# Kernel tuning notes

Measured on AMD Instinct MI355X. Metric: run time of the kernel, lower is better.

## Reference

```python
import jax, jax.numpy as jnp
import numpy as np
from jax import lax

DIM = 256
HEADS = 8
C3 = DIM * 3 // 4  # 192
C1 = DIM // 4      # 64


def conv1x1(x, w):
    # x: [b,c,h,w], w: [o,c] (1x1 conv, no bias)
    return jnp.einsum('bchw,oc->bohw', x, w)


def dwconv3x3(x, w):
    # x: [b,c,h,w], w: [c,1,3,3] depthwise
    return lax.conv_general_dilated(
        x, w, window_strides=(1, 1), padding='SAME',
        feature_group_count=x.shape[1],
        dimension_numbers=('NCHW', 'OIHW', 'NCHW'))


def l2norm(x, eps=1e-12):
    # torch F.normalize: x / max(||x||, eps) along last dim
    n = jnp.sqrt(jnp.sum(x * x, axis=-1, keepdims=True))
    return x / jnp.maximum(n, eps)


def setup_inputs() -> dict:
    key = jax.random.key(0)
    ks = jax.random.split(key, 10)
    s = 0.02
    return {
        'x': jax.random.normal(ks[0], (4, DIM, 128, 128), jnp.float32),
        'k_v': jax.random.normal(ks[1], (4, 256), jnp.float32),
        'temperature': jnp.ones((HEADS, 1, 1), jnp.float32),
        'w_kR': jax.random.normal(ks[2], (C3, 192), jnp.float32) * s,
        'w_kI': jax.random.normal(ks[3], (C1, 64), jnp.float32) * s,
        'w_qR': jax.random.normal(ks[4], (DIM, C3), jnp.float32) * s,
        'w_qdw': jax.random.normal(ks[5], (DIM, 1, 3, 3), jnp.float32) * s,
        'w_kvI': jax.random.normal(ks[6], (2 * DIM, C1), jnp.float32) * s,
        'w_kvdw': jax.random.normal(ks[7], (2 * DIM, 1, 3, 3), jnp.float32) * s,
        'w_proj': jax.random.normal(ks[8], (DIM, DIM), jnp.float32) * s,
    }


def reference(x, k_v, temperature, w_kR, w_kI, w_qR, w_qdw, w_kvI, w_kvdw, w_proj):
    b, c, h, w = x.shape
    # FiLM-style modulation: x * kv + x
    kvr = (k_v[:, :192] @ w_kR.T)[:, :, None, None]  # [b, C3, 1, 1]
    kvi = (k_v[:, 192:] @ w_kI.T)[:, :, None, None]  # [b, C1, 1, 1]
    x_r = x[:, :C3] * kvr + x[:, :C3]
    x_i = x[:, C3:] * kvi + x[:, C3:]
    # QKV projections
    q = dwconv3x3(conv1x1(x_r, w_qR), w_qdw)          # [b, dim, h, w]
    kv = dwconv3x3(conv1x1(x_i, w_kvI), w_kvdw)       # [b, 2*dim, h, w]
    k, v = jnp.split(kv, 2, axis=1)
    hd = DIM // HEADS
    hw = h * w
    q = q.reshape(b, HEADS, hd, hw)
    k = k.reshape(b, HEADS, hd, hw)
    v = v.reshape(b, HEADS, hd, hw)
    # channel-wise (transposed) attention with L2 norm + temperature
    q = l2norm(q)
    k = l2norm(k)
    attn = jnp.einsum('bhcn,bhdn->bhcd', q, k) * temperature  # [b,H,hd,hd]
    attn = jax.nn.softmax(attn, axis=-1)
    out = jnp.einsum('bhcd,bhdn->bhcn', attn, v)
    out = out.reshape(b, DIM, h, w)
    return conv1x1(out, w_proj)
```

## Files before the change

kernel.cpp:

```cpp
#include <hip/hip_runtime.h>
#include <math.h>

#define HW 16384

typedef unsigned int uint;
typedef short bfrag __attribute__((ext_vector_type(8)));
typedef float f32x4 __attribute__((ext_vector_type(4)));

union FragCvt { uint4 u; bfrag v; };

__device__ inline uint pack2bf(float a, float b) {
  uint ua = __builtin_bit_cast(uint, a);
  uint ub = __builtin_bit_cast(uint, b);
  ua = (ua + 0x7FFFu + ((ua >> 16) & 1u)) >> 16;
  ub = (ub + 0x7FFFu + ((ub >> 16) & 1u)) & 0xFFFF0000u;
  return ua | ub;
}

__device__ inline void cvt_hilo(float4 a, float4 b, bfrag& hi, bfrag& lo) {
  float v0[8] = {a.x, a.y, a.z, a.w, b.x, b.y, b.z, b.w};
  uint hv[4], lv[4];
  #pragma unroll
  for (int i = 0; i < 4; ++i) {
    float x0 = v0[2 * i], x1 = v0[2 * i + 1];
    uint h = pack2bf(x0, x1);
    float h0 = __builtin_bit_cast(float, h << 16);
    float h1 = __builtin_bit_cast(float, h & 0xFFFF0000u);
    hv[i] = h;
    lv[i] = pack2bf(x0 - h0, x1 - h1);
  }
  FragCvt ch, cl;
  ch.u = make_uint4(hv[0], hv[1], hv[2], hv[3]);
  cl.u = make_uint4(lv[0], lv[1], lv[2], lv[3]);
  hi = ch.v;
  lo = cl.v;
}

#define LDS_BARRIER() do { \
  asm volatile("s_waitcnt lgkmcnt(0)" ::: "memory"); \
  __builtin_amdgcn_s_barrier(); \
} while (0)

__global__ __launch_bounds__(256) void mod_kernel(
    const float* __restrict__ kv, const float* __restrict__ wkR,
    const float* __restrict__ wkI, float* __restrict__ mod)
{
  int b = blockIdx.x;
  int c = threadIdx.x;
  const float* kvb = kv + b * 256;
  float s = 0.f;
  if (c < 192) {
    const float* wr = wkR + c * 192;
    for (int j = 0; j < 192; ++j) s += kvb[j] * wr[j];
  } else {
    const float* wi = wkI + (c - 192) * 64;
    for (int j = 0; j < 64; ++j) s += kvb[192 + j] * wi[j];
  }
  mod[b * 256 + c] = 1.f + s;
}

__device__ __forceinline__ void mgemm_body(
    const float* __restrict__ Wt, int ldW,
    const float* __restrict__ Xt,
    const float* __restrict__ modc,
    float* __restrict__ Yt,
    int K, int t, unsigned short* Al, unsigned short* Bl, float* Ml)
{
  int w = t >> 6, l = t & 63;
  int wm = (w >> 1) * 64, wn = (w & 1) * 64;
  int lm = l & 15, lk = (l >> 4) * 8;

  int am = t >> 1, ako = (t & 1) * 16;
  int bn = t & 127, bo = (t >> 7) * 8;

  Ml[t] = (modc && t < K) ? modc[t] : 1.f;

  f32x4 acc[4][4];
  #pragma unroll
  for (int fi = 0; fi < 4; ++fi)
    #pragma unroll
    for (int fj = 0; fj < 4; ++fj) acc[fi][fj] = {0.f, 0.f, 0.f, 0.f};

  float xrA[16], xrB[16];
  float4 wv0, wv1, wv2, wv3;

  auto load_x = [&](float* xr, int k0) {
    #pragma unroll
    for (int i = 0; i < 2; ++i) {
      int kb = k0 + bo + i * 16;
      #pragma unroll
      for (int r = 0; r < 8; ++r)
        xr[i * 8 + r] = Xt[(size_t)(kb + r) * HW + bn];
    }
  };
  auto load_w = [&](int k0) {
    const float* wsrc = Wt + (size_t)am * ldW + k0 + ako;
    wv0 = *(const float4*)(wsrc);
    wv1 = *(const float4*)(wsrc + 4);
    wv2 = *(const float4*)(wsrc + 8);
    wv3 = *(const float4*)(wsrc + 12);
  };
  auto pack_a = [&]() {
    uint4 aw0, aw1;
    aw0.x = pack2bf(wv0.x, wv0.y); aw0.y = pack2bf(wv0.z, wv0.w);
    aw0.z = pack2bf(wv1.x, wv1.y); aw0.w = pack2bf(wv1.z, wv1.w);
    aw1.x = pack2bf(wv2.x, wv2.y); aw1.y = pack2bf(wv2.z, wv2.w);
    aw1.z = pack2bf(wv3.x, wv3.y); aw1.w = pack2bf(wv3.z, wv3.w);
    *(uint4*)&Al[am * 40 + ako] = aw0;
    *(uint4*)&Al[am * 40 + ako + 8] = aw1;
  };
  auto pack_b = [&](const float* xr, int k0) {
    #pragma unroll
    for (int i = 0; i < 2; ++i) {
      float4 m0 = *(const float4*)&Ml[k0 + bo + i * 16];
      float4 m1 = *(const float4*)&Ml[k0 + bo + i * 16 + 4];
      uint4 bw;
      bw.x = pack2bf(xr[i * 8 + 0] * m0.x, xr[i * 8 + 1] * m0.y);
      bw.y = pack2bf(xr[i * 8 + 2] * m0.z, xr[i * 8 + 3] * m0.w);
      bw.z = pack2bf(xr[i * 8 + 4] * m1.x, xr[i * 8 + 5] * m1.y);
      bw.w = pack2bf(xr[i * 8 + 6] * m1.z, xr[i * 8 + 7] * m1.w);
      *(uint4*)&Bl[bn * 40 + bo + i * 16] = bw;
    }
  };
  auto mfma_step = [&]() {
    bfrag af[4], bfr[4];
    #pragma unroll
    for (int fj = 0; fj < 4; ++fj) {
      FragCvt cv;
      cv.u = *(const uint4*)&Al[(wm + fj * 16 + lm) * 40 + lk];
      af[fj] = cv.v;
    }
    #pragma unroll
    for (int fi = 0; fi < 4; ++fi) {
      FragCvt cv;
      cv.u = *(const uint4*)&Bl[(wn + fi * 16 + lm) * 40 + lk];
      bfr[fi] = cv.v;
    }
    #pragma unroll
    for (int fi = 0; fi < 4; ++fi)
      #pragma unroll
      for (int fj = 0; fj < 4; ++fj)
        acc[fi][fj] = __builtin_amdgcn_mfma_f32_16x16x32_bf16(
            bfr[fi], af[fj], acc[fi][fj], 0, 0, 0);
  };

  load_x(xrA, 0);
  load_x(xrB, 32);
  load_w(0);

  for (int k0 = 0; k0 < K; k0 += 64) {
    LDS_BARRIER();
    pack_a();
    if (k0 + 32 < K) load_w(k0 + 32);
    pack_b(xrA, k0);
    if (k0 + 64 < K) load_x(xrA, k0 + 64);
    LDS_BARRIER();
    mfma_step();

    LDS_BARRIER();
    pack_a();
    if (k0 + 64 < K) load_w(k0 + 64);
    pack_b(xrB, k0 + 32);
    if (k0 + 96 < K) load_x(xrB, k0 + 96);
    LDS_BARRIER();
    mfma_step();
  }

  int ph = (l >> 4) * 4;
  #pragma unroll
  for (int fi = 0; fi < 4; ++fi)
    #pragma unroll
    for (int fj = 0; fj < 4; ++fj)
      *(f32x4*)&Yt[(size_t)(wm + fj * 16 + lm) * HW + wn + fi * 16 + ph] =
          acc[fi][fj];
}

__global__ __launch_bounds__(256, 2) void mgemm(
    const float* __restrict__ W, int ldW, size_t Wbstride,
    const float* __restrict__ X, int c0, size_t Xbstride,
    const float* __restrict__ mod,
    float* __restrict__ Y, size_t Ybstride, int K)
{
  __shared__ unsigned short Al[128 * 40];
  __shared__ unsigned short Bl[128 * 40];
  __shared__ float Ml[256];
  int b = blockIdx.z, mt = blockIdx.y, nt = blockIdx.x;
  mgemm_body(W + (size_t)b * Wbstride + (size_t)mt * 128 * ldW, ldW,
             X + (size_t)b * Xbstride + (size_t)c0 * HW + nt * 128,
             mod ? mod + b * 256 + c0 : (const float*)nullptr,
             Y + (size_t)b * Ybstride + (size_t)mt * 128 * HW + nt * 128,
             K, threadIdx.x, Al, Bl, Ml);
}

__global__ __launch_bounds__(256, 2) void mgemm_qk(
    const float* __restrict__ wqR, const float* __restrict__ wkvI,
    const float* __restrict__ X, const float* __restrict__ mod,
    float* __restrict__ Yq, float* __restrict__ Yk)
{
  __shared__ unsigned short Al[128 * 40];
  __shared__ unsigned short Bl[128 * 40];
  __shared__ float Ml[256];
  int b = blockIdx.z, mt = blockIdx.y, nt = blockIdx.x;
  if (mt < 2) {
    mgemm_body(wqR + (size_t)mt * 128 * 192, 192,
               X + (size_t)b * 4194304 + nt * 128,
               mod + b * 256,
               Yq + (size_t)b * 4194304 + (size_t)mt * 128 * HW + nt * 128,
               192, threadIdx.x, Al, Bl, Ml);
  } else {
    int m2 = mt - 2;
    mgemm_body(wkvI + (size_t)m2 * 128 * 64, 64,
               X + (size_t)b * 4194304 + (size_t)192 * HW + nt * 128,
               mod + b * 256 + 192,
               Yk + (size_t)b * 4194304 + (size_t)m2 * 128 * HW + nt * 128,
               64, threadIdx.x, Al, Bl, Ml);
  }
}

__global__ __launch_bounds__(256) void dwconv_kernel(
    const float* __restrict__ in, size_t in_bstride,
    const float* __restrict__ wdw,
    float* __restrict__ out, size_t out_bstride,
    float* __restrict__ ssq)
{
  int c = blockIdx.x;
  int b = blockIdx.y;
  int t = threadIdx.x;
  int r = t >> 5;
  int xq = t & 31;

  const float4* ip4 = (const float4*)(in + (size_t)b * in_bstride + ((size_t)c << 14));
  float4* op4 = (float4*)(out + (size_t)b * out_bstride + ((size_t)c << 14));
  const float* wp = wdw + c * 9;
  float w0 = wp[0], w1 = wp[1], w2 = wp[2], w3 = wp[3], w4 = wp[4],
        w5 = wp[5], w6 = wp[6], w7 = wp[7], w8 = wp[8];

  const float4 z4 = make_float4(0.f, 0.f, 0.f, 0.f);
  int y0 = r << 4;

  float4 a = (y0 > 0) ? ip4[((y0 - 1) << 5) + xq] : z4;
  float4 bb = ip4[(y0 << 5) + xq];

  float aL = __shfl_up(a.w, 1);  if (xq == 0)  aL = 0.f;
  float aR = __shfl_down(a.x, 1); if (xq == 31) aR = 0.f;
  float bL = __shfl_up(bb.w, 1); if (xq == 0)  bL = 0.f;
  float bR = __shfl_down(bb.x, 1); if (xq == 31) bR = 0.f;

  float ss = 0.f;
  #pragma unroll
  for (int i = 0; i < 16; ++i) {
    int y = y0 + i;
    int yc = (y + 1 < 128) ? (y + 1) : 127;
    float4 cc = ip4[(yc << 5) + xq];
    if (y + 1 >= 128) { cc.x = 0.f; cc.y = 0.f; cc.z = 0.f; cc.w = 0.f; }
    float cL = __shfl_up(cc.w, 1);  if (xq == 0)  cL = 0.f;
    float cR = __shfl_down(cc.x, 1); if (xq == 31) cR = 0.f;

    float4 o;
    o.x = w0 * aL  + w1 * a.x + w2 * a.y +
          w3 * bL  + w4 * bb.x + w5 * bb.y +
          w6 * cL  + w7 * cc.x + w8 * cc.y;
    o.y = w0 * a.x + w1 * a.y + w2 * a.z +
          w3 * bb.x + w4 * bb.y + w5 * bb.z +
          w6 * cc.x + w7 * cc.y + w8 * cc.z;
    o.z = w0 * a.y + w1 * a.z + w2 * a.w +
          w3 * bb.y + w4 * bb.z + w5 * bb.w +
          w6 * cc.y + w7 * cc.z + w8 * cc.w;
    o.w = w0 * a.z + w1 * a.w + w2 * aR +
          w3 * bb.z + w4 * bb.w + w5 * bR +
          w6 * cc.z + w7 * cc.w + w8 * cR;

    op4[(y << 5) + xq] = o;
    ss += o.x * o.x + o.y * o.y + o.z * o.z + o.w * o.w;

    a = bb; aL = bL; aR = bR;
    bb = cc; bL = cL; bR = cR;
  }

  if (ssq) {
    #pragma unroll
    for (int off = 32; off > 0; off >>= 1) ss += __shfl_down(ss, off);
    __shared__ float red[4];
    if ((t & 63) == 0) red[t >> 6] = ss;
    __syncthreads();
    if (t == 0) ssq[b * 256 + c] = red[0] + red[1] + red[2] + red[3];
  }
}

__global__ __launch_bounds__(256) void gram_kernel(
    const float* __restrict__ qdw, const float* __restrict__ kdw,
    float* __restrict__ S)
{
  int chunk = blockIdx.x, h = blockIdx.y, b = blockIdx.z;
  int t = threadIdx.x;
  int w = t >> 6, l = t & 63;
  int lm = l & 15;
  int lk8 = (l >> 4) * 8;

  const float* qh = qdw + (((size_t)b * 256 + h * 32) << 14);
  const float* kh = kdw + (((size_t)b * 256 + h * 32) << 14);
  const float* q0 = qh + ((size_t)lm << 14);
  const float* q1 = q0 + ((size_t)16 << 14);
  const float* k0 = kh + ((size_t)lm << 14);
  const float* k1 = k0 + ((size_t)16 << 14);

  int px0 = chunk * 1024 + w * 256 + lk8;

  f32x4 acc[2][2], accl[2][2];
  #pragma unroll
  for (int mi = 0; mi < 2; ++mi)
    #pragma unroll
    for (int nj = 0; nj < 2; ++nj) {
      acc[mi][nj] = {0.f, 0.f, 0.f, 0.f};
      accl[mi][nj] = {0.f, 0.f, 0.f, 0.f};
    }

  #pragma unroll 2
  for (int s = 0; s < 8; ++s) {
    int px = px0 + s * 32;
    float4 a0 = *(const float4*)(q0 + px);
    float4 a1 = *(const float4*)(q0 + px + 4);
    float4 a2 = *(const float4*)(q1 + px);
    float4 a3 = *(const float4*)(q1 + px + 4);
    float4 b0 = *(const float4*)(k0 + px);
    float4 b1 = *(const float4*)(k0 + px + 4);
    float4 b2 = *(const float4*)(k1 + px);
    float4 b3 = *(const float4*)(k1 + px + 4);

    bfrag qhF[2], qlF[2], khF[2], klF[2];
    cvt_hilo(a0, a1, qhF[0], qlF[0]);
    cvt_hilo(a2, a3, qhF[1], qlF[1]);
    cvt_hilo(b0, b1, khF[0], klF[0]);
    cvt_hilo(b2, b3, khF[1], klF[1]);

    #pragma unroll
    for (int mi = 0; mi < 2; ++mi)
      #pragma unroll
      for (int nj = 0; nj < 2; ++nj) {
        acc[mi][nj] = __builtin_amdgcn_mfma_f32_16x16x32_bf16(
            qhF[mi], khF[nj], acc[mi][nj], 0, 0, 0);
        accl[mi][nj] = __builtin_amdgcn_mfma_f32_16x16x32_bf16(
            qhF[mi], klF[nj], accl[mi][nj], 0, 0, 0);
        accl[mi][nj] = __builtin_amdgcn_mfma_f32_16x16x32_bf16(
            qlF[mi], khF[nj], accl[mi][nj], 0, 0, 0);
      }
  }

  __shared__ float red[4][1024];
  int orow = (l >> 4) * 4;
  #pragma unroll
  for (int mi = 0; mi < 2; ++mi)
    #pragma unroll
    for (int nj = 0; nj < 2; ++nj)
      #pragma unroll
      for (int r = 0; r < 4; ++r)
        red[w][(mi * 16 + orow + r) * 32 + nj * 16 + lm] =
            acc[mi][nj][r] + accl[mi][nj][r];
  __syncthreads();
  float* Sp = S + (((size_t)b * 8 + h) << 10);
  for (int idx = t; idx < 1024; idx += 256)
    atomicAdd(&Sp[idx], red[0][idx] + red[1][idx] + red[2][idx] + red[3][idx]);
}

__global__ __launch_bounds__(64) void softmax_kernel(
    float* __restrict__ S, const float* __restrict__ ssq,
    const float* __restrict__ ssk, const float* __restrict__ temp)
{
  int bh = blockIdx.x;
  int b = bh >> 3, h = bh & 7;
  int c = threadIdx.x;
  if (c >= 32) return;
  float* row = S + ((size_t)bh << 10) + c * 32;
  float invq = 1.f / fmaxf(sqrtf(ssq[b * 256 + h * 32 + c]), 1e-12f);
  float T = temp[h];
  float lg[32];
  float mx = -1e30f;
  for (int d = 0; d < 32; ++d) {
    float invk = 1.f / fmaxf(sqrtf(ssk[b * 256 + h * 32 + d]), 1e-12f);
    float v = row[d] * invq * invk * T;
    lg[d] = v;
    mx = fmaxf(mx, v);
  }
  float sum = 0.f;
  for (int d = 0; d < 32; ++d) { float e = expf(lg[d] - mx); lg[d] = e; sum += e; }
  float inv = 1.f / sum;
  for (int d = 0; d < 32; ++d) row[d] = lg[d] * inv;
}

__global__ __launch_bounds__(256) void mbuild_kernel(
    const float* __restrict__ attn, const float* __restrict__ wproj,
    float* __restrict__ M)
{
  int o = blockIdx.x, b = blockIdx.y;
  int col = threadIdx.x;
  int h = col >> 5, d = col & 31;
  const float* a = attn + (((size_t)b * 8 + h) << 10);
  const float* wp = wproj + o * 256 + h * 32;
  float s = 0.f;
  #pragma unroll
  for (int cc = 0; cc < 32; ++cc) s += wp[cc] * a[cc * 32 + d];
  M[((size_t)b * 256 + o) * 256 + col] = s;
}

extern "C" void kernel_launch(void* const* d_in, const int* in_sizes, int n_in,
                              void* d_out, int out_size, void* d_ws, size_t ws_size,
                              hipStream_t stream)
{
  const float* x      = (const float*)d_in[0];
  const float* k_v    = (const float*)d_in[1];
  const float* temp   = (const float*)d_in[2];
  const float* w_kR   = (const float*)d_in[3];
  const float* w_kI   = (const float*)d_in[4];
  const float* w_qR   = (const float*)d_in[5];
  const float* w_qdw  = (const float*)d_in[6];
  const float* w_kvI  = (const float*)d_in[7];
  const float* w_kvdw = (const float*)d_in[8];
  const float* w_proj = (const float*)d_in[9];
  float* out = (float*)d_out;

  float* ws   = (float*)d_ws;
  float* bufA = ws;
  float* bufB = ws + 16777216;
  float* bufC = ws + 33554432;
  float* sm   = ws + 50331648;
  float* mod  = sm;
  float* ssq  = sm + 1024;
  float* ssk  = sm + 2048;
  float* S    = sm + 3072;
  float* M    = sm + 3072 + 32768;

  hipMemsetAsync(S, 0, (size_t)32768 * sizeof(float), stream);

  mod_kernel<<<dim3(4), dim3(256), 0, stream>>>(k_v, w_kR, w_kI, mod);

  mgemm_qk<<<dim3(128, 4, 4), dim3(256), 0, stream>>>(
      w_qR, w_kvI, x, mod, bufA, bufB);

  dwconv_kernel<<<dim3(256, 4), dim3(256), 0, stream>>>(
      bufB, 4194304, w_kvdw, bufC, 4194304, ssk);

  dwconv_kernel<<<dim3(256, 4), dim3(256), 0, stream>>>(
      bufA, 4194304, w_qdw, bufB, 4194304, ssq);

  gram_kernel<<<dim3(16, 8, 4), dim3(256), 0, stream>>>(bufB, bufC, S);

  mgemm<<<dim3(128, 2, 4), dim3(256), 0, stream>>>(
      w_kvI + 256 * 64, 64, 0, x, 192, 4194304, mod, bufA, 4194304, 64);

  softmax_kernel<<<dim3(32), dim3(64), 0, stream>>>(S, ssq, ssk, temp);
  mbuild_kernel<<<dim3(256, 4), dim3(256), 0, stream>>>(S, w_proj, M);

  dwconv_kernel<<<dim3(256, 4), dim3(256), 0, stream>>>(
      bufA, 4194304, w_kvdw + 256 * 9, bufC, 4194304, (float*)nullptr);

  mgemm<<<dim3(128, 2, 4), dim3(256), 0, stream>>>(
      M, 256, 65536, bufC, 0, 4194304, (const float*)nullptr, out, 4194304, 256);
}
```

Baseline: 322.7 us.

## Fuse q/k depthwise convolutions and L2 norm sums into the gram kernel

The two depthwise 3x3 convolutions on q and k are computed inside the gram kernel. Each wave now handles one image row and convolves 8-pixel strips directly from the pre-conv buffers, so the dwconv outputs never need to be written to and re-read from memory. The per-channel sum of squares is accumulated in registers and added to ssq/ssk atomically, and one memset now clears those buffers along with S. In exchange, every pre-conv element is loaded three times (once per stencil row, mostly hitting cache), register pressure goes up, and the grid doubles to 32 chunks.

```diff
diff --git a/kernel.cpp b/kernel.cpp
--- a/kernel.cpp
+++ b/kernel.cpp
@@ -287,24 +287,34 @@
   }
 }
 
-__global__ __launch_bounds__(256) void gram_kernel(
-    const float* __restrict__ qdw, const float* __restrict__ kdw,
-    float* __restrict__ S)
+__global__ __launch_bounds__(256, 3) void gram_fused(
+    const float* __restrict__ qpre, const float* __restrict__ kpre,
+    const float* __restrict__ wqdw, const float* __restrict__ wkdw,
+    float* __restrict__ S, float* __restrict__ ssq, float* __restrict__ ssk)
 {
   int chunk = blockIdx.x, h = blockIdx.y, b = blockIdx.z;
   int t = threadIdx.x;
   int w = t >> 6, l = t & 63;
-  int lm = l & 15;
-  int lk8 = (l >> 4) * 8;
-
-  const float* qh = qdw + (((size_t)b * 256 + h * 32) << 14);
-  const float* kh = kdw + (((size_t)b * 256 + h * 32) << 14);
-  const float* q0 = qh + ((size_t)lm << 14);
-  const float* q1 = q0 + ((size_t)16 << 14);
-  const float* k0 = kh + ((size_t)lm << 14);
-  const float* k1 = k0 + ((size_t)16 << 14);
-
-  int px0 = chunk * 1024 + w * 256 + lk8;
+  int lm = l & 15, lk8 = (l >> 4) * 8;
+  int Y = chunk * 4 + w;
+
+  int c0 = h * 32 + lm, c1 = c0 + 16;
+  const float* q0p = qpre + (((size_t)b * 256 + c0) << 14);
+  const float* q1p = qpre + (((size_t)b * 256 + c1) << 14);
+  const float* k0p = kpre + (((size_t)b * 256 + c0) << 14);
+  const float* k1p = kpre + (((size_t)b * 256 + c1) << 14);
+
+  float wq0[9], wq1[9], wk0[9], wk1[9];
+  #pragma unroll
+  for (int j = 0; j < 9; ++j) {
+    wq0[j] = wqdw[c0 * 9 + j]; wq1[j] = wqdw[c1 * 9 + j];
+    wk0[j] = wkdw[c0 * 9 + j]; wk1[j] = wkdw[c1 * 9 + j];
+  }
+
+  bool ym = Y > 0, yp = Y < 127;
+  int r0 = Y << 7;
+  int rm = ym ? r0 - 128 : r0;
+  int rp = yp ? r0 + 128 : r0;
 
   f32x4 acc[2][2], accl[2][2];
   #pragma unroll
@@ -314,24 +324,61 @@
       acc[mi][nj] = {0.f, 0.f, 0.f, 0.f};
       accl[mi][nj] = {0.f, 0.f, 0.f, 0.f};
     }
-
-  #pragma unroll 2
-  for (int s = 0; s < 8; ++s) {
-    int px = px0 + s * 32;
-    float4 a0 = *(const float4*)(q0 + px);
-    float4 a1 = *(const float4*)(q0 + px + 4);
-    float4 a2 = *(const float4*)(q1 + px);
-    float4 a3 = *(const float4*)(q1 + px + 4);
-    float4 b0 = *(const float4*)(k0 + px);
-    float4 b1 = *(const float4*)(k0 + px + 4);
-    float4 b2 = *(const float4*)(k1 + px);
-    float4 b3 = *(const float4*)(k1 + px + 4);
-
+  float nq0 = 0.f, nq1 = 0.f, nk0 = 0.f, nk1 = 0.f;
+
+  auto conv8 = [&](const float* base, const float* wt, int x0, float* o) {
+    float A[3][10];
+    int rows[3] = {rm, r0, rp};
+    #pragma unroll
+    for (int dy = 0; dy < 3; ++dy) {
+      const float* p = base + rows[dy] + x0;
+      float4 m0 = *(const float4*)p;
+      float4 m1 = *(const float4*)(p + 4);
+      int lo = (x0 > 0) ? -1 : 0;
+      int ro = (x0 + 8 < 128) ? 8 : 7;
+      float lv = p[lo];
+      float rv = p[ro];
+      if (x0 == 0) lv = 0.f;
+      if (x0 + 8 >= 128) rv = 0.f;
+      bool valid = (dy == 0) ? ym : ((dy == 2) ? yp : true);
+      if (!valid) {
+        m0 = make_float4(0.f, 0.f, 0.f, 0.f);
+        m1 = make_float4(0.f, 0.f, 0.f, 0.f);
+        lv = 0.f; rv = 0.f;
+      }
+      A[dy][0] = lv;
+      A[dy][1] = m0.x; A[dy][2] = m0.y; A[dy][3] = m0.z; A[dy][4] = m0.w;
+      A[dy][5] = m1.x; A[dy][6] = m1.y; A[dy][7] = m1.z; A[dy][8] = m1.w;
+      A[dy][9] = rv;
+    }
+    #pragma unroll
+    for (int j = 0; j < 8; ++j)
+      o[j] = wt[0] * A[0][j] + wt[1] * A[0][j + 1] + wt[2] * A[0][j + 2] +
+             wt[3] * A[1][j] + wt[4] * A[1][j + 1] + wt[5] * A[1][j + 2] +
+             wt[6] * A[2][j] + wt[7] * A[2][j + 1] + wt[8] * A[2][j + 2];
+  };
+
+  for (int s = 0; s < 4; ++s) {
+    int x0 = lk8 + 32 * s;
+    float oq0[8], oq1[8], ok0[8], ok1[8];
+    conv8(q0p, wq0, x0, oq0);
+    conv8(q1p, wq1, x0, oq1);
+    conv8(k0p, wk0, x0, ok0);
+    conv8(k1p, wk1, x0, ok1);
+    #pragma unroll
+    for (int j = 0; j < 8; ++j) {
+      nq0 += oq0[j] * oq0[j]; nq1 += oq1[j] * oq1[j];
+      nk0 += ok0[j] * ok0[j]; nk1 += ok1[j] * ok1[j];
+    }
     bfrag qhF[2], qlF[2], khF[2], klF[2];
-    cvt_hilo(a0, a1, qhF[0], qlF[0]);
-    cvt_hilo(a2, a3, qhF[1], qlF[1]);
-    cvt_hilo(b0, b1, khF[0], klF[0]);
-    cvt_hilo(b2, b3, khF[1], klF[1]);
+    cvt_hilo(make_float4(oq0[0], oq0[1], oq0[2], oq0[3]),
+             make_float4(oq0[4], oq0[5], oq0[6], oq0[7]), qhF[0], qlF[0]);
+    cvt_hilo(make_float4(oq1[0], oq1[1], oq1[2], oq1[3]),
+             make_float4(oq1[4], oq1[5], oq1[6], oq1[7]), qhF[1], qlF[1]);
+    cvt_hilo(make_float4(ok0[0], ok0[1], ok0[2], ok0[3]),
+             make_float4(ok0[4], ok0[5], ok0[6], ok0[7]), khF[0], klF[0]);
+    cvt_hilo(make_float4(ok1[0], ok1[1], ok1[2], ok1[3]),
+             make_float4(ok1[4], ok1[5], ok1[6], ok1[7]), khF[1], klF[1]);
 
     #pragma unroll
     for (int mi = 0; mi < 2; ++mi)
@@ -344,6 +391,17 @@
         accl[mi][nj] = __builtin_amdgcn_mfma_f32_16x16x32_bf16(
             qlF[mi], khF[nj], accl[mi][nj], 0, 0, 0);
       }
+  }
+
+  nq0 += __shfl_xor(nq0, 16); nq0 += __shfl_xor(nq0, 32);
+  nq1 += __shfl_xor(nq1, 16); nq1 += __shfl_xor(nq1, 32);
+  nk0 += __shfl_xor(nk0, 16); nk0 += __shfl_xor(nk0, 32);
+  nk1 += __shfl_xor(nk1, 16); nk1 += __shfl_xor(nk1, 32);
+  if (l < 16) {
+    atomicAdd(&ssq[b * 256 + c0], nq0);
+    atomicAdd(&ssq[b * 256 + c1], nq1);
+    atomicAdd(&ssk[b * 256 + c0], nk0);
+    atomicAdd(&ssk[b * 256 + c1], nk1);
   }
 
   __shared__ float red[4][1024];
@@ -429,30 +487,25 @@
   float* S    = sm + 3072;
   float* M    = sm + 3072 + 32768;
 
-  hipMemsetAsync(S, 0, (size_t)32768 * sizeof(float), stream);
+  hipMemsetAsync(ssq, 0, (size_t)(1024 + 1024 + 32768) * sizeof(float), stream);
 
   mod_kernel<<<dim3(4), dim3(256), 0, stream>>>(k_v, w_kR, w_kI, mod);
 
   mgemm_qk<<<dim3(128, 4, 4), dim3(256), 0, stream>>>(
       w_qR, w_kvI, x, mod, bufA, bufB);
 
-  dwconv_kernel<<<dim3(256, 4), dim3(256), 0, stream>>>(
-      bufB, 4194304, w_kvdw, bufC, 4194304, ssk);
-
-  dwconv_kernel<<<dim3(256, 4), dim3(256), 0, stream>>>(
-      bufA, 4194304, w_qdw, bufB, 4194304, ssq);
-
-  gram_kernel<<<dim3(16, 8, 4), dim3(256), 0, stream>>>(bufB, bufC, S);
+  gram_fused<<<dim3(32, 8, 4), dim3(256), 0, stream>>>(
+      bufA, bufB, w_qdw, w_kvdw, S, ssq, ssk);
 
   mgemm<<<dim3(128, 2, 4), dim3(256), 0, stream>>>(
-      w_kvI + 256 * 64, 64, 0, x, 192, 4194304, mod, bufA, 4194304, 64);
+      w_kvI + 256 * 64, 64, 0, x, 192, 4194304, mod, bufC, 4194304, 64);
 
   softmax_kernel<<<dim3(32), dim3(64), 0, stream>>>(S, ssq, ssk, temp);
   mbuild_kernel<<<dim3(256, 4), dim3(256), 0, stream>>>(S, w_proj, M);
 
   dwconv_kernel<<<dim3(256, 4), dim3(256), 0, stream>>>(
-      bufA, 4194304, w_kvdw + 256 * 9, bufC, 4194304, (float*)nullptr);
+      bufC, 4194304, w_kvdw + 256 * 9, bufA, 4194304, (float*)nullptr);
 
   mgemm<<<dim3(128, 2, 4), dim3(256), 0, stream>>>(
-      M, 256, 65536, bufC, 0, 4194304, (const float*)nullptr, out, 4194304, 256);
-}
+      M, 256, 65536, bufA, 0, 4194304, (const float*)nullptr, out, 4194304, 256);
+}
```

After: 561.0 us. 1.74x slower.
